# Kernel tuning notes

Measured on AMD Instinct MI355X. Metric: run time of the kernel, lower is better.

The kernel has to match this reference:

```python
import jax, jax.numpy as jnp
import numpy as np

TAU = 2.0          # LIF membrane time constant (init kwarg)
ALPHA = 2.0        # spikingjelly surrogate.ATan default alpha
V_TH = 1.0         # spikingjelly LIFNode default v_threshold

# Heaviside spike with ATan surrogate gradient (spikingjelly semantics)
@jax.custom_vjp
def spike(v):
    return (v >= V_TH).astype(v.dtype)

def _spike_fwd(v):
    return spike(v), v

def _spike_bwd(v, g):
    sg = (ALPHA / 2.0) / (1.0 + (jnp.pi / 2.0 * ALPHA * (v - V_TH)) ** 2)
    return (g * sg,)

spike.defvjp(_spike_fwd, _spike_bwd)

def lif(x):
    # Fresh LIFNode: v_prev = 0, v_reset = 0, decay_input=True
    # charge: v = v_prev + (x - (v_prev - v_reset)) / tau  ->  v = x / tau
    return spike(x / TAU)

def setup_inputs() -> dict:
    key = jax.random.key(0)
    ks = jax.random.split(key, 5)
    B = 2097152
    # kaiming-uniform-ish scale: 1/sqrt(fan_in)
    def w(k, out_f, in_f):
        return jax.random.normal(k, (out_f, in_f), dtype=jnp.float32) / np.sqrt(in_f)
    return {
        "x": jax.random.normal(ks[0], (B, 5), dtype=jnp.float32),
        "W1": w(ks[1], 32, 5),
        "W2": w(ks[2], 32, 32),
        "W3": w(ks[3], 16, 32),
        "W4": w(ks[4], 10, 16),
    }

def reference(x, W1, W2, W3, W4):
    # fc: Linear(5,32)->LIF -> Linear(32,32)->LIF -> Linear(32,16)->LIF
    s = lif(x @ W1.T)          # [B, 32]
    s = lif(s @ W2.T)          # [B, 32]
    s = lif(s @ W3.T)          # [B, 16]
    # fc1: Linear(16,10)->LIF
    return lif(s @ W4.T)       # [B, 10]
```

## Files before the change

kernel.cpp:

```cpp
#include <hip/hip_runtime.h>


typedef float v4f __attribute__((ext_vector_type(4)));

#define RPB 512

__global__ __launch_bounds__(256) void snn_fused(
    const float* __restrict__ x,
    const float* __restrict__ W1,
    const float* __restrict__ W2,
    const float* __restrict__ W3,
    const float* __restrict__ W4,
    float* __restrict__ out,
    int B)
{
    __shared__ float buf[RPB * 10];
    __shared__ float w2t[32 * 36];

    const int t = threadIdx.x;
    const long base = (long)blockIdx.x * RPB;
    const int nrows = (int)min((long)RPB, (long)B - base);

#pragma unroll
    for (int e = t; e < 1024; e += 256) {
        int j = e >> 5, i = e & 31;
        w2t[i * 36 + j] = W2[e];
    }

    if (nrows == RPB) {
        const v4f* xg = (const v4f*)(x + base * 5);
        v4f* b4 = (v4f*)buf;
#pragma unroll
        for (int e = 0; e < 3; ++e) {
            int idx = e * 256 + t;
            if (idx < (RPB * 5) / 4) b4[idx] = xg[idx];
        }
    } else {
        for (int e = t; e < nrows * 5; e += 256) buf[e] = x[base * 5 + e];
    }
    __syncthreads();

    float xr[2][5];
#pragma unroll
    for (int c = 0; c < 2; ++c) {
        int lr = c * 256 + t;
        if (lr < nrows) {
#pragma unroll
            for (int k = 0; k < 5; ++k) xr[c][k] = buf[lr * 5 + k];
        }
    }
    __syncthreads();

#pragma unroll
    for (int c = 0; c < 2; ++c) {
        int lr = c * 256 + t;
        if (lr >= nrows) continue;

        unsigned m = 0u;
#pragma unroll
        for (int j = 0; j < 32; ++j) {
            const float* w = W1 + j * 5;
            float h = xr[c][0] * w[0];
            h += xr[c][1] * w[1];
            h += xr[c][2] * w[2];
            h += xr[c][3] * w[3];
            h += xr[c][4] * w[4];
            if (h >= 2.0f) m |= (1u << j);
        }

        float o[10];
#pragma unroll
        for (int j = 0; j < 10; ++j) o[j] = 0.0f;

        if (m) {
            float h[32];
#pragma unroll
            for (int j = 0; j < 32; ++j) h[j] = 0.0f;
            unsigned mm = m;
            while (mm) {
                int i = __ffs(mm) - 1;
                mm &= mm - 1;
                const float* wr = &w2t[i * 36];
#pragma unroll
                for (int j = 0; j < 32; ++j) h[j] += wr[j];
            }
            unsigned m2 = 0u;
#pragma unroll
            for (int j = 0; j < 32; ++j)
                if (h[j] >= 2.0f) m2 |= (1u << j);

            if (m2) {
                unsigned m3 = 0u;
#pragma unroll
                for (int j = 0; j < 16; ++j) {
                    float g = 0.0f;
#pragma unroll
                    for (int i = 0; i < 32; ++i)
                        if ((m2 >> i) & 1u) g += W3[j * 32 + i];
                    if (g >= 2.0f) m3 |= (1u << j);
                }
#pragma unroll
                for (int j = 0; j < 10; ++j) {
                    float g = 0.0f;
#pragma unroll
                    for (int i = 0; i < 16; ++i)
                        if ((m3 >> i) & 1u) g += W4[j * 16 + i];
                    o[j] = (g >= 2.0f) ? 1.0f : 0.0f;
                }
            }
        }

#pragma unroll
        for (int j = 0; j < 10; ++j) buf[lr * 10 + j] = o[j];
    }
    __syncthreads();

    if (nrows == RPB) {
        v4f* og = (v4f*)(out + base * 10);
        const v4f* b4 = (const v4f*)buf;
#pragma unroll
        for (int e = 0; e < 5; ++e) {
            int idx = e * 256 + t;
            __builtin_nontemporal_store(b4[idx], &og[idx]);
        }
    } else {
        for (int e = t; e < nrows * 10; e += 256) out[base * 10 + e] = buf[e];
    }
}

extern "C" void kernel_launch(void* const* d_in, const int* in_sizes, int n_in,
                              void* d_out, int out_size, void* d_ws, size_t ws_size,
                              hipStream_t stream) {
    const float* x  = (const float*)d_in[0];
    const float* W1 = (const float*)d_in[1];
    const float* W2 = (const float*)d_in[2];
    const float* W3 = (const float*)d_in[3];
    const float* W4 = (const float*)d_in[4];
    float* out = (float*)d_out;

    int B = in_sizes[0] / 5;
    int grid = (B + RPB - 1) / RPB;
    snn_fused<<<grid, 256, 0, stream>>>(x, W1, W2, W3, W4, out, B);
}
```

Before: 144.3 us.

## Add row-max bound early-exit for layer 2 and shrink rows per block

Replaces the shared transposed W2 tile with per-input-column maxima of W2. A thread skips layer 2 and beyond when the popcount times the global max, or the sum of the active column maxima, is below the threshold, since no layer-2 neuron can then fire. Layer 2 now reads W2 straight from global memory. Rows per block drop to 256 (one row per thread), separate input and output buffers are used, and launch bounds request 8 blocks per CU to raise occupancy. The bound test uses a slightly loosened threshold of 1.998 so float rounding does not skip a row that would spike; it adds per-thread cost when many rows pass the test, and the uncached global W2 reads can cost more than the old shared-memory reads.

```diff
diff --git a/kernel.cpp b/kernel.cpp
--- a/kernel.cpp
+++ b/kernel.cpp
@@ -3,9 +3,9 @@
 
 typedef float v4f __attribute__((ext_vector_type(4)));
 
-#define RPB 512
+#define RPB 256
 
-__global__ __launch_bounds__(256) void snn_fused(
+__global__ __launch_bounds__(256, 8) void snn_fused(
     const float* __restrict__ x,
     const float* __restrict__ W1,
     const float* __restrict__ W2,
@@ -14,57 +14,55 @@
     float* __restrict__ out,
     int B)
 {
-    __shared__ float buf[RPB * 10];
-    __shared__ float w2t[32 * 36];
+    __shared__ __align__(16) float xbuf[RPB * 5];
+    __shared__ __align__(16) float obuf[RPB * 10];
+    __shared__ float smx[32];
+    __shared__ float smxmax;
 
     const int t = threadIdx.x;
     const long base = (long)blockIdx.x * RPB;
     const int nrows = (int)min((long)RPB, (long)B - base);
 
+    if (t < 32) {
+        float mm = W2[t];
 #pragma unroll
-    for (int e = t; e < 1024; e += 256) {
-        int j = e >> 5, i = e & 31;
-        w2t[i * 36 + j] = W2[e];
+        for (int j = 1; j < 32; ++j) mm = fmaxf(mm, W2[j * 32 + t]);
+        smx[t] = mm;
+        float r = mm;
+#pragma unroll
+        for (int off = 16; off; off >>= 1) r = fmaxf(r, __shfl_xor(r, off, 32));
+        if (t == 0) smxmax = r;
     }
 
     if (nrows == RPB) {
         const v4f* xg = (const v4f*)(x + base * 5);
-        v4f* b4 = (v4f*)buf;
+        v4f* b4 = (v4f*)xbuf;
 #pragma unroll
-        for (int e = 0; e < 3; ++e) {
+        for (int e = 0; e < 2; ++e) {
             int idx = e * 256 + t;
             if (idx < (RPB * 5) / 4) b4[idx] = xg[idx];
         }
     } else {
-        for (int e = t; e < nrows * 5; e += 256) buf[e] = x[base * 5 + e];
+        for (int e = t; e < nrows * 5; e += 256) xbuf[e] = x[base * 5 + e];
     }
     __syncthreads();
 
-    float xr[2][5];
+    const float mxmax = smxmax;
+
+    if (t < nrows) {
+        float xr[5];
 #pragma unroll
-    for (int c = 0; c < 2; ++c) {
-        int lr = c * 256 + t;
-        if (lr < nrows) {
-#pragma unroll
-            for (int k = 0; k < 5; ++k) xr[c][k] = buf[lr * 5 + k];
-        }
-    }
-    __syncthreads();
-
-#pragma unroll
-    for (int c = 0; c < 2; ++c) {
-        int lr = c * 256 + t;
-        if (lr >= nrows) continue;
+        for (int k = 0; k < 5; ++k) xr[k] = xbuf[t * 5 + k];
 
         unsigned m = 0u;
 #pragma unroll
         for (int j = 0; j < 32; ++j) {
             const float* w = W1 + j * 5;
-            float h = xr[c][0] * w[0];
-            h += xr[c][1] * w[1];
-            h += xr[c][2] * w[2];
-            h += xr[c][3] * w[3];
-            h += xr[c][4] * w[4];
+            float h = xr[0] * w[0];
+            h += xr[1] * w[1];
+            h += xr[2] * w[2];
+            h += xr[3] * w[3];
+            h += xr[4] * w[4];
             if (h >= 2.0f) m |= (1u << j);
         }
 
@@ -72,59 +70,65 @@
 #pragma unroll
         for (int j = 0; j < 10; ++j) o[j] = 0.0f;
 
-        if (m) {
-            float h[32];
+        if ((float)__popc(m) * mxmax >= 1.998f) {
+            float S = 0.0f;
+            unsigned mm = m;
+            while (mm) { int i = __ffs(mm) - 1; mm &= mm - 1; S += smx[i]; }
+            if (S >= 1.998f) {
+                float h2[32];
 #pragma unroll
-            for (int j = 0; j < 32; ++j) h[j] = 0.0f;
-            unsigned mm = m;
-            while (mm) {
-                int i = __ffs(mm) - 1;
-                mm &= mm - 1;
-                const float* wr = &w2t[i * 36];
+                for (int j = 0; j < 32; ++j) h2[j] = 0.0f;
+                mm = m;
+                while (mm) {
+                    int i = __ffs(mm) - 1;
+                    mm &= mm - 1;
+                    const float* col = W2 + i;
 #pragma unroll
-                for (int j = 0; j < 32; ++j) h[j] += wr[j];
-            }
-            unsigned m2 = 0u;
+                    for (int j = 0; j < 32; ++j) h2[j] += col[j * 32];
+                }
+                unsigned m2 = 0u;
 #pragma unroll
-            for (int j = 0; j < 32; ++j)
-                if (h[j] >= 2.0f) m2 |= (1u << j);
+                for (int j = 0; j < 32; ++j)
+                    if (h2[j] >= 2.0f) m2 |= (1u << j);
 
-            if (m2) {
-                unsigned m3 = 0u;
+                if (m2) {
+                    unsigned m3 = 0u;
 #pragma unroll
-                for (int j = 0; j < 16; ++j) {
-                    float g = 0.0f;
+                    for (int j = 0; j < 16; ++j) {
+                        float g = 0.0f;
 #pragma unroll
-                    for (int i = 0; i < 32; ++i)
-                        if ((m2 >> i) & 1u) g += W3[j * 32 + i];
-                    if (g >= 2.0f) m3 |= (1u << j);
-                }
+                        for (int i = 0; i < 32; ++i)
+                            if ((m2 >> i) & 1u) g += W3[j * 32 + i];
+                        if (g >= 2.0f) m3 |= (1u << j);
+                    }
 #pragma unroll
-                for (int j = 0; j < 10; ++j) {
-                    float g = 0.0f;
+                    for (int j = 0; j < 10; ++j) {
+                        float g = 0.0f;
 #pragma unroll
-                    for (int i = 0; i < 16; ++i)
-                        if ((m3 >> i) & 1u) g += W4[j * 16 + i];
-                    o[j] = (g >= 2.0f) ? 1.0f : 0.0f;
+                        for (int i = 0; i < 16; ++i)
+                            if ((m3 >> i) & 1u) g += W4[j * 16 + i];
+                        o[j] = (g >= 2.0f) ? 1.0f : 0.0f;
+                    }
                 }
             }
         }
 
 #pragma unroll
-        for (int j = 0; j < 10; ++j) buf[lr * 10 + j] = o[j];
+        for (int j = 0; j < 10; ++j) obuf[t * 10 + j] = o[j];
     }
     __syncthreads();
 
     if (nrows == RPB) {
         v4f* og = (v4f*)(out + base * 10);
-        const v4f* b4 = (const v4f*)buf;
+        const v4f* b4 = (const v4f*)obuf;
 #pragma unroll
-        for (int e = 0; e < 5; ++e) {
+        for (int e = 0; e < 3; ++e) {
             int idx = e * 256 + t;
-            __builtin_nontemporal_store(b4[idx], &og[idx]);
+            if (idx < (RPB * 10) / 4)
+                __builtin_nontemporal_store(b4[idx], &og[idx]);
         }
     } else {
-        for (int e = t; e < nrows * 10; e += 256) out[base * 10 + e] = buf[e];
+        for (int e = t; e < nrows * 10; e += 256) out[base * 10 + e] = obuf[e];
     }
 }
 
```

After: 156.7 us. +8.6%, slower.
